# Performance work log

Measured on AMD Instinct MI355X. Metric: run time of the kernel, lower is better.

## Reference

```python
import jax, jax.numpy as jnp
import numpy as np

HIDDEN = 1280
HEADS = 16
HEAD_DIM = HIDDEN // HEADS  # 80
INTER = 4608
DEPTH = 4
WIN = 64                     # tokens per attention window
FULL_BLOCKS = (3,)           # fullatt_block_indexes
EPS = 1e-6
SEQ = 3072


def setup_inputs() -> dict:
    key = jax.random.key(0)
    ks = jax.random.split(key, 20)
    sc = lambda *s: 0.02
    inp = {
        "x": jax.random.normal(ks[0], (SEQ, HIDDEN), jnp.float32),
        "rotary_pos_emb": jax.random.uniform(ks[1], (SEQ, HEAD_DIM // 2), jnp.float32) * 3.0,
        "s_aux": jax.random.normal(ks[2], (HEADS,), jnp.float32),
        "ln1_w": jnp.ones((DEPTH, HIDDEN), jnp.float32),
        "ln1_b": jnp.zeros((DEPTH, HIDDEN), jnp.float32),
        "qkv_w": jax.random.normal(ks[3], (DEPTH, HIDDEN, 3 * HIDDEN), jnp.float32) * 0.02,
        "qkv_b": jnp.zeros((DEPTH, 3 * HIDDEN), jnp.float32),
        "proj_w": jax.random.normal(ks[4], (DEPTH, HIDDEN, HIDDEN), jnp.float32) * 0.02,
        "proj_b": jnp.zeros((DEPTH, HIDDEN), jnp.float32),
        "ln2_w": jnp.ones((DEPTH, HIDDEN), jnp.float32),
        "ln2_b": jnp.zeros((DEPTH, HIDDEN), jnp.float32),
        "gate_w": jax.random.normal(ks[5], (DEPTH, HIDDEN, INTER), jnp.float32) * 0.02,
        "gate_b": jnp.zeros((DEPTH, INTER), jnp.float32),
        "up_w": jax.random.normal(ks[6], (DEPTH, HIDDEN, INTER), jnp.float32) * 0.02,
        "up_b": jnp.zeros((DEPTH, INTER), jnp.float32),
        "down_w": jax.random.normal(ks[7], (DEPTH, INTER, HIDDEN), jnp.float32) * 0.02,
        "down_b": jnp.zeros((DEPTH, HIDDEN), jnp.float32),
    }
    return inp


def _layer_norm(x, w, b):
    mu = jnp.mean(x, axis=-1, keepdims=True)
    var = jnp.mean(jnp.square(x - mu), axis=-1, keepdims=True)
    return (x - mu) * jax.lax.rsqrt(var + EPS) * w + b


def _rotate_half(x):
    x1, x2 = jnp.split(x, 2, axis=-1)
    return jnp.concatenate([-x2, x1], axis=-1)


def _apply_rotary(q, k, rot):
    # q,k: [S, H, D]; rot: [S, D/2]
    emb = jnp.concatenate([rot, rot], axis=-1)          # [S, D]
    cos = jnp.cos(emb)[:, None, :]
    sin = jnp.sin(emb)[:, None, :]
    q = q * cos + _rotate_half(q) * sin
    k = k * cos + _rotate_half(k) * sin
    return q, k


def _attention_with_sinks(q, k, v, s_aux):
    # q,k,v: [B, T, H, D]; block-diagonal within each of B windows.
    scale = 1.0 / jnp.sqrt(jnp.asarray(HEAD_DIM, q.dtype))
    scores = jnp.einsum("bqhd,bkhd->bhqk", q, k) * scale      # [B,H,q,k]
    sink = s_aux[None, :, None]                                # [1,H,1]
    m = jnp.maximum(jnp.max(scores, axis=-1), sink)            # [B,H,q]
    p = jnp.exp(scores - m[..., None])                         # [B,H,q,k]
    denom = jnp.sum(p, axis=-1) + jnp.exp(sink - m)            # [B,H,q]
    out = jnp.einsum("bhqk,bkhd->bqhd", p, v)
    out = out / jnp.transpose(denom, (0, 2, 1))[..., None]     # [B,q,H,D]
    return out


def reference(x, rotary_pos_emb, s_aux, ln1_w, ln1_b, qkv_w, qkv_b, proj_w, proj_b,
              ln2_w, ln2_b, gate_w, gate_b, up_w, up_b, down_w, down_b):
    S = x.shape[0]
    h = x
    for l in range(DEPTH):
        # --- attention ---
        hn = _layer_norm(h, ln1_w[l], ln1_b[l])
        qkv = hn @ qkv_w[l] + qkv_b[l]                          # [S, 3*HIDDEN]
        qkv = qkv.reshape(S, 3, HEADS, HEAD_DIM)
        q, k, v = qkv[:, 0], qkv[:, 1], qkv[:, 2]               # [S,H,D]
        q, k = _apply_rotary(q, k, rotary_pos_emb)
        if l in FULL_BLOCKS:
            B, T = 1, S                                         # full attention
        else:
            B, T = S // WIN, WIN                                # windowed (varlen block-diag)
        qw = q.reshape(B, T, HEADS, HEAD_DIM)
        kw = k.reshape(B, T, HEADS, HEAD_DIM)
        vw = v.reshape(B, T, HEADS, HEAD_DIM)
        o = _attention_with_sinks(qw, kw, vw, s_aux)            # [B,T,H,D]
        o = o.reshape(S, HIDDEN) @ proj_w[l] + proj_b[l]
        h = h + o
        # --- gated SiLU MLP ---
        hn = _layer_norm(h, ln2_w[l], ln2_b[l])
        g = jax.nn.silu(hn @ gate_w[l] + gate_b[l]) * (hn @ up_w[l] + up_b[l])
        h = h + g @ down_w[l] + down_b[l]
    return h
```

## Files before the change

kernel.cpp:

```cpp
#include <hip/hip_runtime.h>
#include <math.h>

typedef unsigned short u16;
typedef unsigned int u32;

using bf16x8 = __attribute__((ext_vector_type(8))) __bf16;
using f32x4  = __attribute__((ext_vector_type(4))) float;

#define SEQ 3072
#define HID 1280
#define NHEADS 16
#define HDIM 80
#define INTER 4608

#define LOG2E 1.44269504088896f
#define M2C   11.5415603f

__device__ __forceinline__ u16 f2bf(float f) {
    __bf16 h = (__bf16)f;
    return __builtin_bit_cast(u16, h);
}

__device__ __forceinline__ void gld16(const void* g, void* l) {
    __builtin_amdgcn_global_load_lds((const __attribute__((address_space(1))) void*)g,
                                     (__attribute__((address_space(3))) void*)l,
                                     16, 0, 0);
}

__device__ __forceinline__ bf16x8 frag8(const u16* base, int row, int ks, int quad) {
    int c = ks * 4 + quad;
    return *(const bf16x8*)&base[(row * 8 + (c ^ (row & 7))) * 8];
}

__global__ __launch_bounds__(256) void transpose_pack(const float* __restrict__ src,
                                                      u16* __restrict__ dst, int K, int N) {
    __shared__ float tile[32][33];
    int l = blockIdx.z;
    const float* s = src + (size_t)l * K * N;
    u16* d = dst + (size_t)l * N * K;
    int n0 = blockIdx.x * 32, k0 = blockIdx.y * 32;
    int tx = threadIdx.x & 31, ty = threadIdx.x >> 5;
#pragma unroll
    for (int i = 0; i < 4; i++) {
        int k = ty + i * 8;
        tile[k][tx] = s[(size_t)(k0 + k) * N + n0 + tx];
    }
    __syncthreads();
#pragma unroll
    for (int i = 0; i < 4; i++) {
        int n = ty + i * 8;
        d[(size_t)(n0 + n) * K + k0 + tx] = f2bf(tile[tx][n]);
    }
}

__global__ __launch_bounds__(256) void transpose_pack_gu(const float* __restrict__ src,
                                                         u16* __restrict__ dst, int K, int N,
                                                         int which) {
    __shared__ float tile[32][33];
    int l = blockIdx.z;
    const float* s = src + (size_t)l * K * N;
    u16* d = dst + (size_t)l * (2 * N) * K;
    int n0 = blockIdx.x * 32, k0 = blockIdx.y * 32;
    int tx = threadIdx.x & 31, ty = threadIdx.x >> 5;
#pragma unroll
    for (int i = 0; i < 4; i++) {
        int k = ty + i * 8;
        tile[k][tx] = s[(size_t)(k0 + k) * N + n0 + tx];
    }
    __syncthreads();
#pragma unroll
    for (int i = 0; i < 4; i++) {
        int n = ty + i * 8;
        int g = n0 + n;
        int n2 = ((g >> 4) << 5) | (g & 15) | (which << 4);
        d[(size_t)n2 * K + k0 + tx] = f2bf(tile[tx][n]);
    }
}

__global__ __launch_bounds__(256) void ln_kernel(const float* __restrict__ x,
                                                 const float* __restrict__ w,
                                                 const float* __restrict__ b,
                                                 u16* __restrict__ out) {
    int row = blockIdx.x;
    const float* xr = x + (size_t)row * HID;
    float v[5]; float s = 0.f, s2 = 0.f;
#pragma unroll
    for (int i = 0; i < 5; i++) { float t = xr[threadIdx.x + i * 256]; v[i] = t; s += t; s2 += t * t; }
#pragma unroll
    for (int off = 32; off > 0; off >>= 1) { s += __shfl_down(s, off); s2 += __shfl_down(s2, off); }
    __shared__ float red[8];
    int wv = threadIdx.x >> 6;
    if ((threadIdx.x & 63) == 0) { red[wv] = s; red[wv + 4] = s2; }
    __syncthreads();
    s  = red[0] + red[1] + red[2] + red[3];
    s2 = red[4] + red[5] + red[6] + red[7];
    float mu  = s * (1.f / HID);
    float var = s2 * (1.f / HID) - mu * mu;
    float rstd = rsqrtf(var + 1e-6f);
#pragma unroll
    for (int i = 0; i < 5; i++) {
        int col = threadIdx.x + i * 256;
        out[(size_t)row * HID + col] = f2bf((v[i] - mu) * rstd * w[col] + b[col]);
    }
}

__global__ __launch_bounds__(256) void qkv_pack(const float* __restrict__ qkv,
                                                const float* __restrict__ rot,
                                                u16* __restrict__ Qp, u16* __restrict__ Kp,
                                                u16* __restrict__ Vt) {
    const float QSC = 0.111803398874989485f * LOG2E;
    int s0 = blockIdx.x * 64, h = blockIdx.y;
    int tid = threadIdx.x;
    __shared__ u16 vlds[80 * 66];
    for (int idx = tid; idx < 64 * 40; idx += 256) {
        int r = idx / 40, d = idx - r * 40;
        const float* base = qkv + (size_t)(s0 + r) * 3840 + h * 80;
        float sn, cs;
        __sincosf(rot[(size_t)(s0 + r) * 40 + d], &sn, &cs);
        float q1 = base[d], q2 = base[d + 40];
        float k1 = base[1280 + d], k2 = base[1280 + d + 40];
        size_t ro = ((size_t)h * SEQ + s0 + r) * 128;
        Qp[ro + d]      = f2bf((q1 * cs - q2 * sn) * QSC);
        Qp[ro + d + 40] = f2bf((q2 * cs + q1 * sn) * QSC);
        Kp[ro + d]      = f2bf(k1 * cs - k2 * sn);
        Kp[ro + d + 40] = f2bf(k2 * cs + k1 * sn);
    }
    for (int idx = tid; idx < 64 * 48; idx += 256) {
        int r = idx / 48, d = 80 + (idx - r * 48);
        size_t ro = ((size_t)h * SEQ + s0 + r) * 128;
        Qp[ro + d] = 0; Kp[ro + d] = 0;
    }
    for (int idx = tid; idx < 64 * 80; idx += 256) {
        int r = idx / 80, d = idx - r * 80;
        vlds[d * 66 + r] = f2bf(qkv[(size_t)(s0 + r) * 3840 + 2560 + h * 80 + d]);
    }
    __syncthreads();
    for (int idx = tid; idx < 80 * 64; idx += 256) {
        int d = idx >> 6, ky = idx & 63;
        Vt[((size_t)h * 80 + d) * SEQ + s0 + ky] = vlds[d * 66 + ky];
    }
}

template<int BM, int EPI>
__global__ __launch_bounds__(512, 2) void gemm8(const u16* __restrict__ A,
                                                const u16* __restrict__ B,
                                                const float* __restrict__ bias0,
                                                const float* __restrict__ bias1,
                                                const float* __restrict__ res,
                                                float* __restrict__ outf,
                                                u16* __restrict__ outh,
                                                int N, int K) {
    constexpr int MT   = 3072 / BM;
    constexpr int MF   = BM / 32;
    constexpr int LA   = BM / 64;
    constexpr int LT   = LA + 2;
    constexpr int ABUF = BM * 64;
    constexpr int BUFU = ABUF + 8192;
    __shared__ u16 sbuf[3 * BUFU];

    int tid = threadIdx.x, lane = tid & 63, wave = tid >> 6;
    int quad = lane >> 4, r15 = lane & 15;
    int wm = wave >> 2, wn = wave & 3;

    int nwg = gridDim.x;
    int q8 = nwg >> 3, r8 = nwg & 7;
    int xcd = blockIdx.x & 7, j = blockIdx.x >> 3;
    int wg = (xcd < r8 ? xcd * (q8 + 1) : r8 * (q8 + 1) + (xcd - r8) * q8) + j;
    int bx = wg / MT, by = wg % MT;
    int mBase = by * BM, nBase = bx * 128;

    int rs = tid >> 3, cs = tid & 7;
    int c0 = cs ^ (rs & 7);
    const u16* gA = A + (size_t)(mBase + rs) * K + c0 * 8;
    const u16* gB = B + (size_t)(nBase + rs) * K + c0 * 8;
    int nK = K >> 6;

    f32x4 acc[MF][2] = {};

    auto stage1 = [&](int kt, int jl) {
        int b = kt % 3;
        if (jl < LA) {
            gld16(gA + (size_t)kt * 64 + (size_t)(jl * 64) * K,
                  &sbuf[b * BUFU + jl * 4096 + wave * 512]);
        } else {
            int i = jl - LA;
            gld16(gB + (size_t)kt * 64 + (size_t)(i * 64) * K,
                  &sbuf[b * BUFU + ABUF + i * 4096 + wave * 512]);
        }
    };

#pragma unroll
    for (int jl = 0; jl < LT; jl++) stage1(0, jl);
#pragma unroll
    for (int jl = 0; jl < LT; jl++) stage1(1, jl);
    if constexpr (BM == 256) asm volatile("s_waitcnt vmcnt(6)" ::: "memory");
    else                     asm volatile("s_waitcnt vmcnt(4)" ::: "memory");
    __builtin_amdgcn_s_barrier();

    for (int kt = 0; kt < nK; kt++) {
        const u16* Ab = &sbuf[(kt % 3) * BUFU];
        const u16* Bb = Ab + ABUF;
        bool pre = (kt + 2 < nK);
#pragma unroll
        for (int ks = 0; ks < 2; ks++) {
            bf16x8 af[MF], bf[2];
#pragma unroll
            for (int mi = 0; mi < MF; mi++)
                af[mi] = frag8(Ab, wm * (BM / 2) + mi * 16 + r15, ks, quad);
#pragma unroll
            for (int ni = 0; ni < 2; ni++)
                bf[ni] = frag8(Bb, wn * 32 + ni * 16 + r15, ks, quad);
            if (pre) {
#pragma unroll
                for (int jl = 0; jl < LT / 2; jl++) stage1(kt + 2, ks * (LT / 2) + jl);
            }
            __builtin_amdgcn_s_barrier();
            __builtin_amdgcn_s_setprio(1);
#pragma unroll
            for (int mi = 0; mi < MF; mi++)
#pragma unroll
                for (int ni = 0; ni < 2; ni++)
                    acc[mi][ni] = __builtin_amdgcn_mfma_f32_16x16x32_bf16(
                        af[mi], bf[ni], acc[mi][ni], 0, 0, 0);
            __builtin_amdgcn_s_setprio(0);
            if (ks == 0) __builtin_amdgcn_s_barrier();
        }
        if (pre) {
            if constexpr (BM == 256) asm volatile("s_waitcnt vmcnt(6)" ::: "memory");
            else                     asm volatile("s_waitcnt vmcnt(4)" ::: "memory");
        } else if (kt + 1 < nK) {
            asm volatile("s_waitcnt vmcnt(0)" ::: "memory");
        }
        __builtin_amdgcn_s_barrier();
    }

    if constexpr (EPI == 2) {
        int col = (nBase >> 1) + wn * 16 + r15;
        float gb = bias0[col], ub = bias1[col];
#pragma unroll
        for (int mi = 0; mi < MF; mi++)
#pragma unroll
            for (int jj = 0; jj < 4; jj++) {
                int row = mBase + wm * (BM / 2) + mi * 16 + quad * 4 + jj;
                float g = acc[mi][0][jj] + gb;
                float u = acc[mi][1][jj] + ub;
                float sg = g / (1.f + __expf(-g));
                outh[(size_t)row * INTER + col] = f2bf(sg * u);
            }
    } else {
#pragma unroll
        for (int ni = 0; ni < 2; ni++) {
            int col = nBase + wn * 32 + ni * 16 + r15;
            float bv = bias0[col];
#pragma unroll
            for (int mi = 0; mi < MF; mi++)
#pragma unroll
                for (int jj = 0; jj < 4; jj++) {
                    int row = mBase + wm * (BM / 2) + mi * 16 + quad * 4 + jj;
                    float v = acc[mi][ni][jj] + bv;
                    if constexpr (EPI == 1) v += res[(size_t)row * N + col];
                    outf[(size_t)row * N + col] = v;
                }
        }
    }
}

template<int QR>
__global__ __launch_bounds__(256) void attn_kernel(const u16* __restrict__ Qp,
                                                   const u16* __restrict__ Kp,
                                                   const u16* __restrict__ Vt,
                                                   const float* __restrict__ s_aux,
                                                   u16* __restrict__ out) {
    constexpr int MH = QR / 64;
    __shared__ u16 q_lds[QR * 128];
    __shared__ u16 k_lds[8192];
    __shared__ u16 v_lds[5120];
    __shared__ u16 p_lds[QR * 72];

    int qt = blockIdx.x, h = blockIdx.y;
    int tid = threadIdx.x, lane = tid & 63, wave = tid >> 6;
    int quad = lane >> 4, r15 = lane & 15;

    const u16* Qh = Qp + (size_t)h * SEQ * 128;
    const u16* Kh = Kp + (size_t)h * SEQ * 128;
    const u16* Vh = Vt + (size_t)h * 80 * SEQ;

    {
        int q0 = qt * QR;
#pragma unroll
        for (int i = 0; i < QR / 16; i++) {
            int slot = i * 256 + tid;
            int row = slot >> 4, cc = slot & 15;
            int c = cc ^ (row & 7);
            gld16(Qh + (size_t)(q0 + row) * 128 + c * 8, &q_lds[(i * 256 + wave * 64) * 8]);
        }
    }
    __syncthreads();
    bf16x8 aq[MH][3];
#pragma unroll
    for (int mh = 0; mh < MH; mh++)
#pragma unroll
        for (int ks = 0; ks < 3; ks++) {
            int row = wave * (16 * MH) + mh * 16 + r15;
            int c = ks * 4 + quad;
            aq[mh][ks] = *(const bf16x8*)&q_lds[(row * 16 + (c ^ (row & 7))) * 8];
        }

    float l_j[MH][4] = {};
    f32x4 ov[MH][5] = {};

    int nT = (QR == 64) ? 1 : (SEQ / 64);
    int tBase = (QR == 64) ? qt : 0;
    for (int t = 0; t < nT; t++) {
        int key0 = (tBase + t) * 64;
        __syncthreads();
#pragma unroll
        for (int i = 0; i < 4; i++) {
            int slot = i * 256 + wave * 64 + lane;
            int row = slot >> 4, cc = slot & 15;
            int c = cc ^ (row & 7);
            gld16(Kh + (size_t)(key0 + row) * 128 + c * 8, &k_lds[(i * 256 + wave * 64) * 8]);
        }
#pragma unroll
        for (int i = 0; i < 2; i++) {
            int slot = i * 256 + wave * 64 + lane;
            int row = slot >> 3, cc = slot & 7;
            int c = cc ^ (row & 7);
            gld16(Vh + (size_t)row * SEQ + key0 + c * 8, &v_lds[(i * 256 + wave * 64) * 8]);
        }
        if (wave < 2) {
            int slot = 512 + wave * 64 + lane;
            int row = slot >> 3, cc = slot & 7;
            int c = cc ^ (row & 7);
            gld16(Vh + (size_t)row * SEQ + key0 + c * 8, &v_lds[(512 + wave * 64) * 8]);
        }
        __syncthreads();

        f32x4 sc[MH][4] = {};
#pragma unroll
        for (int nt = 0; nt < 4; nt++)
#pragma unroll
            for (int ks = 0; ks < 3; ks++) {
                int row = nt * 16 + r15;
                int c = ks * 4 + quad;
                bf16x8 bk = *(const bf16x8*)&k_lds[(row * 16 + (c ^ (row & 7))) * 8];
#pragma unroll
                for (int mh = 0; mh < MH; mh++)
                    sc[mh][nt] = __builtin_amdgcn_mfma_f32_16x16x32_bf16(aq[mh][ks], bk, sc[mh][nt], 0, 0, 0);
            }
#pragma unroll
        for (int mh = 0; mh < MH; mh++)
#pragma unroll
            for (int nt = 0; nt < 4; nt++)
#pragma unroll
                for (int jj = 0; jj < 4; jj++) {
                    float p = __builtin_amdgcn_exp2f(sc[mh][nt][jj] - M2C);
                    l_j[mh][jj] += p;
                    p_lds[(wave * 16 * MH + mh * 16 + quad * 4 + jj) * 72 + nt * 16 + r15] = f2bf(p);
                }
        asm volatile("s_waitcnt lgkmcnt(0)" ::: "memory");
        bf16x8 ap[MH][2];
#pragma unroll
        for (int mh = 0; mh < MH; mh++)
#pragma unroll
            for (int ks = 0; ks < 2; ks++)
                ap[mh][ks] = *(const bf16x8*)&p_lds[(wave * 16 * MH + mh * 16 + r15) * 72 + ks * 32 + quad * 8];
#pragma unroll
        for (int t5 = 0; t5 < 5; t5++)
#pragma unroll
            for (int ks = 0; ks < 2; ks++) {
                int d = t5 * 16 + r15;
                int c = ks * 4 + quad;
                bf16x8 bv = *(const bf16x8*)&v_lds[(d * 8 + (c ^ (d & 7))) * 8];
#pragma unroll
                for (int mh = 0; mh < MH; mh++)
                    ov[mh][t5] = __builtin_amdgcn_mfma_f32_16x16x32_bf16(ap[mh][ks], bv, ov[mh][t5], 0, 0, 0);
            }
    }
#pragma unroll
    for (int mh = 0; mh < MH; mh++)
#pragma unroll
        for (int off = 1; off < 16; off <<= 1)
#pragma unroll
            for (int jj = 0; jj < 4; jj++)
                l_j[mh][jj] += __shfl_xor(l_j[mh][jj], off, 64);
    float sink = s_aux[h];
    float se = __builtin_amdgcn_exp2f(sink * LOG2E - M2C);
#pragma unroll
    for (int mh = 0; mh < MH; mh++)
#pragma unroll
        for (int jj = 0; jj < 4; jj++) l_j[mh][jj] = 1.f / (l_j[mh][jj] + se);
#pragma unroll
    for (int mh = 0; mh < MH; mh++)
#pragma unroll
        for (int t5 = 0; t5 < 5; t5++)
#pragma unroll
            for (int jj = 0; jj < 4; jj++) {
                int row = qt * QR + wave * 16 * MH + mh * 16 + quad * 4 + jj;
                int d = t5 * 16 + r15;
                out[(size_t)row * HID + h * 80 + d] = f2bf(ov[mh][t5][jj] * l_j[mh][jj]);
            }
}

__global__ __launch_bounds__(256) void copy4_kernel(const float4* __restrict__ src,
                                                    float4* __restrict__ dst) {
    size_t i = (size_t)blockIdx.x * 256 + threadIdx.x;
    dst[i] = src[i];
}

extern "C" void kernel_launch(void* const* d_in, const int* in_sizes, int n_in,
                              void* d_out, int out_size, void* d_ws, size_t ws_size,
                              hipStream_t stream) {
    const float* x      = (const float*)d_in[0];
    const float* rot    = (const float*)d_in[1];
    const float* s_aux  = (const float*)d_in[2];
    const float* ln1_w  = (const float*)d_in[3];
    const float* ln1_b  = (const float*)d_in[4];
    const float* qkv_w  = (const float*)d_in[5];
    const float* qkv_b  = (const float*)d_in[6];
    const float* proj_w = (const float*)d_in[7];
    const float* proj_b = (const float*)d_in[8];
    const float* ln2_w  = (const float*)d_in[9];
    const float* ln2_b  = (const float*)d_in[10];
    const float* gate_w = (const float*)d_in[11];
    const float* gate_b = (const float*)d_in[12];
    const float* up_w   = (const float*)d_in[13];
    const float* up_b   = (const float*)d_in[14];
    const float* down_w = (const float*)d_in[15];
    const float* down_b = (const float*)d_in[16];

    char* ws = (char*)d_ws;
    size_t off = 0;
    auto alloc = [&](size_t n) -> char* {
        char* p = ws + off; off += (n + 255) & ~(size_t)255; return p;
    };
    u16* wt_qkv  = (u16*)alloc((size_t)4 * 3840 * 1280 * 2);
    u16* wt_proj = (u16*)alloc((size_t)4 * 1280 * 1280 * 2);
    u16* wt_gu   = (u16*)alloc((size_t)4 * 9216 * 1280 * 2);
    u16* wt_down = (u16*)alloc((size_t)4 * 1280 * 4608 * 2);
    float* h     = (float*)alloc((size_t)3072 * 1280 * 4);
    u16*  xn     = (u16*)alloc((size_t)3072 * 1280 * 2);
    float* gbuf  = (float*)alloc((size_t)3072 * 4608 * 4);
    float* qkvb  = gbuf;
    u16*  attnb  = (u16*)alloc((size_t)3072 * 1280 * 2);
    float* ubuf  = (float*)alloc((size_t)3072 * 4608 * 4);
    u16*  mbuf   = (u16*)alloc((size_t)3072 * 4608 * 2);
    u16* Qp  = (u16*)ubuf;
    u16* Kp  = Qp + (size_t)NHEADS * SEQ * 128;
    u16* Vtp = Kp + (size_t)NHEADS * SEQ * 128;

    transpose_pack<<<dim3(120, 40, 4), 256, 0, stream>>>(qkv_w,  wt_qkv,  1280, 3840);
    transpose_pack<<<dim3(40,  40, 4), 256, 0, stream>>>(proj_w, wt_proj, 1280, 1280);
    transpose_pack_gu<<<dim3(144, 40, 4), 256, 0, stream>>>(gate_w, wt_gu, 1280, 4608, 0);
    transpose_pack_gu<<<dim3(144, 40, 4), 256, 0, stream>>>(up_w,   wt_gu, 1280, 4608, 1);
    transpose_pack<<<dim3(40, 144, 4), 256, 0, stream>>>(down_w, wt_down, 4608, 1280);

    copy4_kernel<<<3840, 256, 0, stream>>>((const float4*)x, (float4*)h);

    for (int l = 0; l < 4; l++) {
        ln_kernel<<<3072, 256, 0, stream>>>(h, ln1_w + l * 1280, ln1_b + l * 1280, xn);
        gemm8<256, 0><<<360, 512, 0, stream>>>(xn, wt_qkv + (size_t)l * 3840 * 1280,
                                               qkv_b + l * 3840, nullptr, nullptr,
                                               qkvb, nullptr, 3840, 1280);
        qkv_pack<<<dim3(48, 16), 256, 0, stream>>>(qkvb, rot, Qp, Kp, Vtp);
        if (l == 3)
            attn_kernel<128><<<dim3(SEQ / 128, 16), 256, 0, stream>>>(Qp, Kp, Vtp, s_aux, attnb);
        else
            attn_kernel<64><<<dim3(SEQ / 64, 16), 256, 0, stream>>>(Qp, Kp, Vtp, s_aux, attnb);
        gemm8<128, 1><<<240, 512, 0, stream>>>(attnb, wt_proj + (size_t)l * 1280 * 1280,
                                               proj_b + l * 1280, nullptr, h,
                                               h, nullptr, 1280, 1280);
        ln_kernel<<<3072, 256, 0, stream>>>(h, ln2_w + l * 1280, ln2_b + l * 1280, xn);
        gemm8<256, 2><<<864, 512, 0, stream>>>(xn, wt_gu + (size_t)l * 9216 * 1280,
                                               gate_b + l * 4608, up_b + l * 4608, nullptr,
                                               nullptr, mbuf, 9216, 1280);
        float* outp = (l == 3) ? (float*)d_out : h;
        gemm8<128, 1><<<240, 512, 0, stream>>>(mbuf, wt_down + (size_t)l * 4608 * 1280,
                                               down_b + l * 1280, nullptr, h,
                                               outp, nullptr, 1280, 4608);
    }
}
```

Baseline: 1.557 ms.

## Add 192x256-tile GEMM kernel for QKV and gate/up projections

Introduces a new GEMM kernel with a 192x256 output tile per workgroup (6x4 MFMA fragments per wave), double-buffered A and triple-buffered B staging, and an XCD-aware block remap. It replaces the previous 256-row-tile kernel for the QKV and fused gate/up projections, cutting the grid from 360 to 240 and from 864 to 576 workgroups. Each workgroup now does more MFMA work per LDS fragment load. The cost is higher register pressure from the larger accumulator array and a smaller grid, which can leave some CUs idle.

Measured after the change: 1.467 ms. -5.8%, faster.

```diff
diff --git a/kernel.cpp b/kernel.cpp
--- a/kernel.cpp
+++ b/kernel.cpp
@@ -141,6 +141,118 @@
     }
 }
 
+template<int EPI>
+__global__ __launch_bounds__(512, 2) void gemm256(const u16* __restrict__ A,
+                                                  const u16* __restrict__ B,
+                                                  const float* __restrict__ bias0,
+                                                  const float* __restrict__ bias1,
+                                                  float* __restrict__ outf,
+                                                  u16* __restrict__ outh,
+                                                  int N, int K) {
+    __shared__ u16 sbuf[73728];
+    int tid = threadIdx.x, lane = tid & 63, wave = tid >> 6;
+    int quad = lane >> 4, r15 = lane & 15;
+    int wm = wave >> 2, wn = wave & 3;
+
+    int nwg = gridDim.x;
+    int q8 = nwg >> 3, r8 = nwg & 7;
+    int xcd = blockIdx.x & 7, j = blockIdx.x >> 3;
+    int wg = (xcd < r8 ? xcd * (q8 + 1) : r8 * (q8 + 1) + (xcd - r8) * q8) + j;
+    int bx = wg >> 4, by = wg & 15;
+    int mBase = by * 192, nBase = bx * 256;
+
+    int rs = tid >> 3, cs = tid & 7;
+    int c0 = cs ^ (rs & 7);
+    const u16* gA = A + (size_t)(mBase + rs) * K + c0 * 8;
+    const u16* gB = B + (size_t)(nBase + rs) * K + c0 * 8;
+    int nK = K >> 6;
+
+    f32x4 acc[6][4] = {};
+
+    auto stageA = [&](int kt, int jl) {
+        gld16(gA + (size_t)kt * 64 + (size_t)(jl * 64) * K,
+              &sbuf[(kt & 1) * 12288 + jl * 4096 + wave * 512]);
+    };
+    auto stageB = [&](int kt, int jl) {
+        gld16(gB + (size_t)kt * 64 + (size_t)(jl * 64) * K,
+              &sbuf[24576 + (kt % 3) * 16384 + jl * 4096 + wave * 512]);
+    };
+
+#pragma unroll
+    for (int jl = 0; jl < 3; jl++) stageA(0, jl);
+#pragma unroll
+    for (int jl = 0; jl < 4; jl++) stageB(0, jl);
+#pragma unroll
+    for (int jl = 0; jl < 4; jl++) stageB(1, jl);
+    asm volatile("s_waitcnt vmcnt(4)" ::: "memory");
+    __builtin_amdgcn_s_barrier();
+
+    for (int kt = 0; kt < nK; kt++) {
+        const u16* Ab = &sbuf[(kt & 1) * 12288];
+        const u16* Bb = &sbuf[24576 + (kt % 3) * 16384];
+        bool preA = (kt + 1 < nK), preB = (kt + 2 < nK);
+#pragma unroll
+        for (int ks = 0; ks < 2; ks++) {
+            bf16x8 af[6], bf[4];
+#pragma unroll
+            for (int mi = 0; mi < 6; mi++)
+                af[mi] = frag8(Ab, wm * 96 + mi * 16 + r15, ks, quad);
+#pragma unroll
+            for (int ni = 0; ni < 4; ni++)
+                bf[ni] = frag8(Bb, wn * 64 + ni * 16 + r15, ks, quad);
+            if (ks == 0) {
+                if (preA) { stageA(kt + 1, 0); stageA(kt + 1, 1); stageA(kt + 1, 2); }
+            } else {
+                if (preB) { stageB(kt + 2, 0); stageB(kt + 2, 1); stageB(kt + 2, 2); stageB(kt + 2, 3); }
+            }
+            __builtin_amdgcn_s_barrier();
+            __builtin_amdgcn_s_setprio(1);
+#pragma unroll
+            for (int mi = 0; mi < 6; mi++)
+#pragma unroll
+                for (int ni = 0; ni < 4; ni++)
+                    acc[mi][ni] = __builtin_amdgcn_mfma_f32_16x16x32_bf16(
+                        af[mi], bf[ni], acc[mi][ni], 0, 0, 0);
+            __builtin_amdgcn_s_setprio(0);
+            if (ks == 0) __builtin_amdgcn_s_barrier();
+        }
+        if (preB)      { asm volatile("s_waitcnt vmcnt(4)" ::: "memory"); }
+        else if (preA) { asm volatile("s_waitcnt vmcnt(0)" ::: "memory"); }
+        __builtin_amdgcn_s_barrier();
+    }
+
+    if constexpr (EPI == 0) {
+#pragma unroll
+        for (int ni = 0; ni < 4; ni++) {
+            int col = nBase + wn * 64 + ni * 16 + r15;
+            float bv = bias0[col];
+#pragma unroll
+            for (int a = 0; a < 6; a++)
+#pragma unroll
+                for (int jj = 0; jj < 4; jj++) {
+                    int row = mBase + wm * 96 + a * 16 + quad * 4 + jj;
+                    outf[(size_t)row * N + col] = acc[a][ni][jj] + bv;
+                }
+        }
+    } else {
+#pragma unroll
+        for (int pp = 0; pp < 2; pp++) {
+            int col = (nBase >> 1) + wn * 32 + pp * 16 + r15;
+            float gb = bias0[col], ub = bias1[col];
+#pragma unroll
+            for (int a = 0; a < 6; a++)
+#pragma unroll
+                for (int jj = 0; jj < 4; jj++) {
+                    int row = mBase + wm * 96 + a * 16 + quad * 4 + jj;
+                    float g = acc[a][2 * pp][jj] + gb;
+                    float u = acc[a][2 * pp + 1][jj] + ub;
+                    float sg = g / (1.f + __expf(-g));
+                    outh[(size_t)row * INTER + col] = f2bf(sg * u);
+                }
+        }
+    }
+}
+
 template<int BM, int EPI>
 __global__ __launch_bounds__(512, 2) void gemm8(const u16* __restrict__ A,
                                                 const u16* __restrict__ B,
@@ -193,8 +305,7 @@
     for (int jl = 0; jl < LT; jl++) stage1(0, jl);
 #pragma unroll
     for (int jl = 0; jl < LT; jl++) stage1(1, jl);
-    if constexpr (BM == 256) asm volatile("s_waitcnt vmcnt(6)" ::: "memory");
-    else                     asm volatile("s_waitcnt vmcnt(4)" ::: "memory");
+    asm volatile("s_waitcnt vmcnt(4)" ::: "memory");
     __builtin_amdgcn_s_barrier();
 
     for (int kt = 0; kt < nK; kt++) {
@@ -226,42 +337,26 @@
             if (ks == 0) __builtin_amdgcn_s_barrier();
         }
         if (pre) {
-            if constexpr (BM == 256) asm volatile("s_waitcnt vmcnt(6)" ::: "memory");
-            else                     asm volatile("s_waitcnt vmcnt(4)" ::: "memory");
+            asm volatile("s_waitcnt vmcnt(4)" ::: "memory");
         } else if (kt + 1 < nK) {
             asm volatile("s_waitcnt vmcnt(0)" ::: "memory");
         }
         __builtin_amdgcn_s_barrier();
     }
 
-    if constexpr (EPI == 2) {
-        int col = (nBase >> 1) + wn * 16 + r15;
-        float gb = bias0[col], ub = bias1[col];
+#pragma unroll
+    for (int ni = 0; ni < 2; ni++) {
+        int col = nBase + wn * 32 + ni * 16 + r15;
+        float bv = bias0[col];
 #pragma unroll
         for (int mi = 0; mi < MF; mi++)
 #pragma unroll
             for (int jj = 0; jj < 4; jj++) {
                 int row = mBase + wm * (BM / 2) + mi * 16 + quad * 4 + jj;
-                float g = acc[mi][0][jj] + gb;
-                float u = acc[mi][1][jj] + ub;
-                float sg = g / (1.f + __expf(-g));
-                outh[(size_t)row * INTER + col] = f2bf(sg * u);
+                float v = acc[mi][ni][jj] + bv;
+                if constexpr (EPI == 1) v += res[(size_t)row * N + col];
+                outf[(size_t)row * N + col] = v;
             }
-    } else {
-#pragma unroll
-        for (int ni = 0; ni < 2; ni++) {
-            int col = nBase + wn * 32 + ni * 16 + r15;
-            float bv = bias0[col];
-#pragma unroll
-            for (int mi = 0; mi < MF; mi++)
-#pragma unroll
-                for (int jj = 0; jj < 4; jj++) {
-                    int row = mBase + wm * (BM / 2) + mi * 16 + quad * 4 + jj;
-                    float v = acc[mi][ni][jj] + bv;
-                    if constexpr (EPI == 1) v += res[(size_t)row * N + col];
-                    outf[(size_t)row * N + col] = v;
-                }
-        }
     }
 }
 
@@ -459,9 +554,9 @@
 
     for (int l = 0; l < 4; l++) {
         ln_kernel<<<3072, 256, 0, stream>>>(h, ln1_w + l * 1280, ln1_b + l * 1280, xn);
-        gemm8<256, 0><<<360, 512, 0, stream>>>(xn, wt_qkv + (size_t)l * 3840 * 1280,
-                                               qkv_b + l * 3840, nullptr, nullptr,
-                                               qkvb, nullptr, 3840, 1280);
+        gemm256<0><<<240, 512, 0, stream>>>(xn, wt_qkv + (size_t)l * 3840 * 1280,
+                                            qkv_b + l * 3840, nullptr,
+                                            qkvb, nullptr, 3840, 1280);
         qkv_pack<<<dim3(48, 16), 256, 0, stream>>>(qkvb, rot, Qp, Kp, Vtp);
         if (l == 3)
             attn_kernel<128><<<dim3(SEQ / 128, 16), 256, 0, stream>>>(Qp, Kp, Vtp, s_aux, attnb);
@@ -471,9 +566,9 @@
                                                proj_b + l * 1280, nullptr, h,
                                                h, nullptr, 1280, 1280);
         ln_kernel<<<3072, 256, 0, stream>>>(h, ln2_w + l * 1280, ln2_b + l * 1280, xn);
-        gemm8<256, 2><<<864, 512, 0, stream>>>(xn, wt_gu + (size_t)l * 9216 * 1280,
-                                               gate_b + l * 4608, up_b + l * 4608, nullptr,
-                                               nullptr, mbuf, 9216, 1280);
+        gemm256<2><<<576, 512, 0, stream>>>(xn, wt_gu + (size_t)l * 9216 * 1280,
+                                            gate_b + l * 4608, up_b + l * 4608,
+                                            nullptr, mbuf, 9216, 1280);
         float* outp = (l == 3) ? (float*)d_out : h;
         gemm8<128, 1><<<240, 512, 0, stream>>>(mbuf, wt_down + (size_t)l * 4608 * 1280,
                                                down_b + l * 1280, nullptr, h,
```
